# Performance work log

Measured on AMD Instinct MI355X. Metric: run time of the kernel, lower is better.

The kernel has to match this reference:

```python
import jax, jax.numpy as jnp
import numpy as np

MUL0, MUL1 = 128, 64            # scalar (0e) and vector (1o) multiplicities
B = 8192                        # batch of nodes
SQRT3 = 3.0 ** 0.5
SQRT6 = 6.0 ** 0.5

# path normalization (e3nn 'component' irrep norm / 'element' path norm):
# coeff_ins = sqrt(dim(ir_out) / fan_in(i_out)), fan_in = sum_{ins -> i_out} mul1*mul2
A_0E = (1.0 / (MUL0 * MUL0 + MUL1 * MUL1)) ** 0.5   # paths (0,0,0)+(1,1,0)
A_1O = (3.0 / (MUL0 * MUL1 + MUL1 * MUL0)) ** 0.5   # paths (0,1,1)+(1,0,1)
A_1E = (3.0 / (MUL1 * MUL1)) ** 0.5                  # path  (1,1,1)


def _levi_civita():
    eps = np.zeros((3, 3, 3), dtype=np.float32)
    eps[0, 1, 2] = eps[1, 2, 0] = eps[2, 0, 1] = 1.0
    eps[0, 2, 1] = eps[2, 1, 0] = eps[1, 0, 2] = -1.0
    return jnp.asarray(eps)


def setup_inputs() -> dict:
    key = jax.random.key(0)
    ks = jax.random.split(key, 7)
    return {
        "x1": jax.random.normal(ks[0], (B, MUL0 + 3 * MUL1), dtype=jnp.float32),
        "x2": jax.random.normal(ks[1], (B, MUL0 + 3 * MUL1), dtype=jnp.float32),
        "w000": jax.random.normal(ks[2], (MUL0, MUL0, MUL0), dtype=jnp.float32),
        "w011": jax.random.normal(ks[3], (MUL0, MUL1, MUL1), dtype=jnp.float32),
        "w101": jax.random.normal(ks[4], (MUL1, MUL0, MUL1), dtype=jnp.float32),
        "w110": jax.random.normal(ks[5], (MUL1, MUL1, MUL0), dtype=jnp.float32),
        "w111": jax.random.normal(ks[6], (MUL1, MUL1, MUL1), dtype=jnp.float32),
    }


def reference(x1, x2, w000, w011, w101, w110, w111):
    b = x1.shape[0]
    # split irreps: scalars [b, 128], vectors [b, 64, 3]
    s1, v1 = x1[:, :MUL0], x1[:, MUL0:].reshape(b, MUL1, 3)
    s2, v2 = x2[:, :MUL0], x2[:, MUL0:].reshape(b, MUL1, 3)

    # 0e output: 0e x 0e -> 0e (w3j = 1) and 1o x 1o -> 0e (w3j = delta/sqrt3)
    out0 = A_0E * (
        jnp.einsum("uvw,bu,bv->bw", w000, s1, s2)
        + jnp.einsum("uvw,bui,bvi->bw", w110, v1, v2) / SQRT3
    )

    # 1o output: 0e x 1o -> 1o and 1o x 0e -> 1o (w3j = delta/sqrt3)
    out1o = (A_1O / SQRT3) * (
        jnp.einsum("uvw,bu,bvi->bwi", w011, s1, v2)
        + jnp.einsum("uvw,bui,bv->bwi", w101, v1, s2)
    )

    # 1e output: 1o x 1o -> 1e (w3j = levi-civita / sqrt6)
    eps = _levi_civita()
    out1e = (A_1E / SQRT6) * jnp.einsum("uvw,bui,bvj,ijk->bwk", w111, v1, v2, eps)

    return jnp.concatenate(
        [out0, out1o.reshape(b, -1), out1e.reshape(b, -1)], axis=-1
    )  # [b, 128 + 192 + 192] = [b, 512]
```

## Files before the change

### kernel.cpp

```cpp
#include <hip/hip_runtime.h>
#include <stdint.h>


typedef _Float16 f16;
typedef f16 f16x8 __attribute__((ext_vector_type(8)));
typedef float f32x4 __attribute__((ext_vector_type(4)));
typedef int i32x4 __attribute__((ext_vector_type(4)));

#define OFF_W000 0u
#define OFF_W110 2097152u
#define OFF_W011 2621440u
#define OFF_W101 3145728u
#define OFF_W111 3670016u
#define OFF_XS1  3932160u
#define OFF_XS2  4980736u
#define OFF_XV1  6029312u
#define OFF_XV2  7602176u
#define OFF_S0A  9175040u
#define OFF_S0B  10223616u
#define OFF_S1O  13369344u
#define WS_ELEMS 14942208u

#define SC_0E 0.006987712429686843f
#define SC_1O 0.0078125f
#define SC_1E 0.011048543456039806f

__global__ void tile_weights_k(const float* __restrict__ w000, const float* __restrict__ w011,
                               const float* __restrict__ w101, const float* __restrict__ w110,
                               const float* __restrict__ w111, f16* __restrict__ ws)
{
  unsigned tid = blockIdx.x*256u + threadIdx.x;
  if (tid < 2097152u) {
    unsigned e=tid&7u, n=(tid>>3)&127u, q=(tid>>10)&3u, p=(tid>>12)&1u, u=(tid>>13)&127u, vh=(tid>>20)&1u;
    unsigned v = vh*64u + p*32u + q*8u + e;
    ws[OFF_W000+tid] = (f16)w000[u*16384u + v*128u + n];
    return;
  }
  tid -= 2097152u;
  if (tid < 524288u) {
    unsigned e=tid&7u, n=(tid>>3)&127u, q=(tid>>10)&3u, p=(tid>>12)&1u, u=tid>>13;
    unsigned v = p*32u + q*8u + e;
    ws[OFF_W110+tid] = (f16)(w110[u*8192u + v*128u + n] * 0.5773502691896258f);
    return;
  }
  tid -= 524288u;
  if (tid < 524288u) {
    unsigned e=tid&7u, n=(tid>>3)&63u, q=(tid>>9)&3u, p=(tid>>11)&1u, u=tid>>12;
    unsigned v = p*32u + q*8u + e;
    ws[OFF_W011+tid] = (f16)w011[u*4096u + v*64u + n];
    return;
  }
  tid -= 524288u;
  if (tid < 524288u) {
    unsigned e=tid&7u, n=(tid>>3)&63u, q=(tid>>9)&3u, p=(tid>>11)&1u, u=tid>>12;
    unsigned v = p*32u + q*8u + e;
    ws[OFF_W101+tid] = (f16)w101[v*8192u + u*64u + n];
    return;
  }
  tid -= 524288u;
  {
    unsigned e=tid&7u, n=(tid>>3)&63u, q=(tid>>9)&3u, p=(tid>>11)&1u, u=tid>>12;
    unsigned v = p*32u + q*8u + e;
    ws[OFF_W111+tid] = (f16)w111[u*4096u + v*64u + n];
  }
}

__global__ void tile_x_k(const float* __restrict__ x1, const float* __restrict__ x2,
                         f16* __restrict__ ws)
{
  unsigned tid = blockIdx.x*256u + threadIdx.x;
  if (tid < 1048576u) {
    unsigned e=tid&7u, r=(tid>>3)&127u, uo=(tid>>10)&15u, rt=tid>>14;
    ws[OFF_XS1+tid] = (f16)x1[(rt*128u+r)*320u + uo*8u + e];
    return;
  }
  tid -= 1048576u;
  if (tid < 1572864u) {
    unsigned e=tid&7u, r=(tid>>3)&127u, ov=(tid>>10)&7u, rest=tid>>13;
    unsigned i=rest%3u, rt=rest/3u;
    ws[OFF_XV1+tid] = (f16)x1[(rt*128u+r)*320u + 128u + (ov*8u+e)*3u + i];
    return;
  }
  tid -= 1572864u;
  if (tid < 1048576u) {
    unsigned e=tid&7u, r=(tid>>3)&127u, uo=(tid>>10)&15u, rt=tid>>14;
    ws[OFF_XS2+tid] = (f16)x2[(rt*128u+r)*320u + uo*8u + e];
    return;
  }
  tid -= 1048576u;
  {
    unsigned e=tid&7u, r=(tid>>3)&127u, ov=(tid>>10)&7u, rest=tid>>13;
    unsigned i=rest%3u, rt=rest/3u;
    ws[OFF_XV2+tid] = (f16)x2[(rt*128u+r)*320u + 128u + (ov*8u+e)*3u + i];
  }
}

#define GLD16(g,l) __builtin_amdgcn_global_load_lds( \
    (const __attribute__((address_space(1))) unsigned int*)(g), \
    (__attribute__((address_space(3))) unsigned int*)(l), 16, 0, 0)

#define WAITV(n) asm volatile("s_waitcnt vmcnt(" #n ")" ::: "memory")

template<int N, bool NEG>
__device__ __forceinline__ void run_phase(const f16* __restrict__ Wt, int supersteps,
    const f16* __restrict__ aW, const f16* __restrict__ bW, int bRow, int h,
    f16* sW, f16* sA, f32x4 (&acc)[4][4])
{
  constexpr int S = N/64;
  constexpr int TILE = N*32;
  const int lane = threadIdx.x & 63, wid = threadIdx.x >> 6;
  const int q = lane >> 4, r15 = lane & 15;
  const int steps = supersteps*16;

  f16x8 br[4][2];
#pragma unroll
  for (int mt=0; mt<4; ++mt)
#pragma unroll
    for (int o=0; o<2; ++o)
      br[mt][o] = *(const f16x8*)(bW + (o*4+q)*1024 + (bRow + mt*16 + r15)*8);
#pragma unroll
  for (int mt=0; mt<4; ++mt)
#pragma unroll
    for (int o=0; o<2; ++o) {
      i32x4 tmp = __builtin_bit_cast(i32x4, br[mt][o]);
      asm volatile("" :: "v"(tmp));
    }

  auto stW = [&](int t, int buf){
#pragma unroll
    for (int c=0;c<S;++c)
      GLD16((const char*)(Wt + t*TILE + (wid*S+c)*512) + lane*16,
            (char*)(sW + buf*4096 + (wid*S+c)*512));
  };
  auto stA = [&](int uo, int buf){
    GLD16((const char*)(aW + uo*1024) + lane*16, (char*)(sA + buf*512));
  };

  stW(0,0); stA(0,0); stW(1,1);
  asm volatile("s_waitcnt vmcnt(0)" ::: "memory");
  __builtin_amdgcn_s_barrier();
  __builtin_amdgcn_sched_barrier(0);

  int rb = 0;
  for (int ss = 0; ss < supersteps; ++ss) {
    const f16* ab = sA + (ss&1)*512;
#pragma unroll
    for (int p = 0; p < 16; ++p) {
      const int t = ss*16 + p;
      if (t + 2 < steps) {
        if (p >= 14) { if constexpr (S==1) WAITV(2); else WAITV(3); }
        else         { if constexpr (S==1) WAITV(1); else WAITV(2); }
      } else WAITV(0);
      __builtin_amdgcn_s_barrier();
      __builtin_amdgcn_sched_barrier(0);
      int wb = rb+2; if (wb>=3) wb-=3;
      if (t + 2 < steps) stW(t+2, wb);
      if (p == 13 && ss+1 < supersteps) stA(ss+1, (ss+1)&1);

      const int ul = p>>1, par = p&1;
      f16x8 af[4];
#pragma unroll
      for (int mt=0; mt<4; ++mt) {
        f16 av = ab[(mt*16+r15)*8 + ul];
        if constexpr (NEG) av = -av;
        af[mt] = av * br[mt][par];
      }
      const f16* W = sW + rb*4096;
#pragma unroll
      for (int nt=0; nt<4; ++nt) {
        f16x8 bw = *(const f16x8*)(W + (q*N + h*64 + nt*16 + r15)*8);
#pragma unroll
        for (int mt=0; mt<4; ++mt)
          acc[mt][nt] = __builtin_amdgcn_mfma_f32_16x16x32_f16(af[mt], bw, acc[mt][nt], 0,0,0);
      }
      rb = rb+1; if (rb>=3) rb-=3;
    }
  }
  __builtin_amdgcn_s_barrier();
  __builtin_amdgcn_sched_barrier(0);
}

__global__ __launch_bounds__(256, 3)
void tp_main(f16* __restrict__ ws, float* __restrict__ out)
{
  __shared__ f16 smem[16384];
  f16* sW = smem;
  const int lane = threadIdx.x & 63, wid = threadIdx.x >> 6;
  f16* sA = smem + 12288 + wid*1024;
  const int q = lane >> 4, r15 = lane & 15;

  f32x4 acc[4][4];
#pragma unroll
  for (int a=0;a<4;++a)
#pragma unroll
    for (int b=0;b<4;++b) acc[a][b] = (f32x4){0.f,0.f,0.f,0.f};

  const int bid = blockIdx.x;

  if (bid < 128) {
    const int rt = bid >> 1, vh = bid & 1;
    const int rgrp = wid >> 1, h = wid & 1;
    const f16* aW = ws + OFF_XS1 + rt*16384 + rgrp*512;
    const f16* bW = ws + OFF_XS2 + rt*16384 + vh*8192;
    run_phase<128,false>(ws + OFF_W000 + vh*1048576u, 16, aW, bW, rgrp*64, h, sW, sA, acc);
    const int rowb = rt*128 + rgrp*64;
    if (vh == 0) {
#pragma unroll
      for (int mt=0;mt<4;++mt)
#pragma unroll
        for (int nt=0;nt<4;++nt)
#pragma unroll
          for (int rg=0;rg<4;++rg)
            out[(rowb+mt*16+q*4+rg)*512 + h*64+nt*16+r15] = SC_0E*acc[mt][nt][rg];
    } else {
      f16* slab = ws + OFF_S0A;
#pragma unroll
      for (int mt=0;mt<4;++mt)
#pragma unroll
        for (int nt=0;nt<4;++nt)
#pragma unroll
          for (int rg=0;rg<4;++rg)
            slab[(rowb+mt*16+q*4+rg)*128 + h*64+nt*16+r15] = (f16)(SC_0E*acc[mt][nt][rg]);
    }
  } else if (bid < 224) {
    const int id = bid-128, i = id%3, rt = id/3;
    const int rgrp = wid, ro = rgrp & 1, sub = rgrp >> 1;
    const int rtt = rt*2 + sub;
    const f16* aW = ws + OFF_XS1 + rtt*16384 + ro*512;
    const f16* bW = ws + OFF_XV2 + (rtt*3+i)*8192;
    run_phase<64,false>(ws + OFF_W011, 16, aW, bW, ro*64, 0, sW, sA, acc);
    const int rowb = rt*256 + rgrp*64;
#pragma unroll
    for (int mt=0;mt<4;++mt)
#pragma unroll
      for (int nt=0;nt<4;++nt)
#pragma unroll
        for (int rg=0;rg<4;++rg)
          out[(rowb+mt*16+q*4+rg)*512 + 128 + 3*(nt*16+r15) + i] = SC_1O*acc[mt][nt][rg];
  } else if (bid < 320) {
    const int id = bid-224, i = id%3, rt = id/3;
    const int rgrp = wid, ro = rgrp & 1, sub = rgrp >> 1;
    const int rtt = rt*2 + sub;
    const f16* aW = ws + OFF_XS2 + rtt*16384 + ro*512;
    const f16* bW = ws + OFF_XV1 + (rtt*3+i)*8192;
    run_phase<64,false>(ws + OFF_W101, 16, aW, bW, ro*64, 0, sW, sA, acc);
    const int rowb = rt*256 + rgrp*64;
    f16* slab = ws + OFF_S1O;
#pragma unroll
    for (int mt=0;mt<4;++mt)
#pragma unroll
      for (int nt=0;nt<4;++nt)
#pragma unroll
        for (int rg=0;rg<4;++rg)
          slab[(rowb+mt*16+q*4+rg)*192 + 3*(nt*16+r15) + i] = (f16)(SC_1O*acc[mt][nt][rg]);
  } else if (bid < 416) {
    const int id = bid-320, kk = id%3, rt = id/3;
    int i = kk+1; if (i>2) i-=3;
    int j = kk+2; if (j>2) j-=3;
    const int rgrp = wid, ro = rgrp & 1, sub = rgrp >> 1;
    const int rtt = rt*2 + sub;
    run_phase<64,false>(ws + OFF_W111, 8,
        ws + OFF_XV1 + (rtt*3+i)*8192 + ro*512, ws + OFF_XV2 + (rtt*3+j)*8192,
        ro*64, 0, sW, sA, acc);
    run_phase<64,true>(ws + OFF_W111, 8,
        ws + OFF_XV1 + (rtt*3+j)*8192 + ro*512, ws + OFF_XV2 + (rtt*3+i)*8192,
        ro*64, 0, sW, sA, acc);
    const int rowb = rt*256 + rgrp*64;
#pragma unroll
    for (int mt=0;mt<4;++mt)
#pragma unroll
      for (int nt=0;nt<4;++nt)
#pragma unroll
        for (int rg=0;rg<4;++rg)
          out[(rowb+mt*16+q*4+rg)*512 + 320 + 3*(nt*16+r15) + kk] = SC_1E*acc[mt][nt][rg];
  } else {
    const int id = bid-416, i = id%3, rt = id/3;
    const int rgrp = wid >> 1, h = wid & 1;
    const f16* aW = ws + OFF_XV1 + (rt*3+i)*8192 + rgrp*512;
    const f16* bW = ws + OFF_XV2 + (rt*3+i)*8192;
    run_phase<128,false>(ws + OFF_W110, 8, aW, bW, rgrp*64, h, sW, sA, acc);
    const int rowb = rt*128 + rgrp*64;
    f16* slab = ws + OFF_S0B + (unsigned)i*1048576u;
#pragma unroll
    for (int mt=0;mt<4;++mt)
#pragma unroll
      for (int nt=0;nt<4;++nt)
#pragma unroll
        for (int rg=0;rg<4;++rg)
          slab[(rowb+mt*16+q*4+rg)*128 + h*64+nt*16+r15] = (f16)(SC_0E*acc[mt][nt][rg]);
  }
}

__global__ void ep_add(const f16* __restrict__ ws, float* __restrict__ out)
{
  unsigned tid = blockIdx.x*256u + threadIdx.x;
  if (tid < 1048576u) {
    unsigned r = tid>>7, c = tid&127u;
    float s = (float)ws[OFF_S0A+tid] + (float)ws[OFF_S0B+tid]
            + (float)ws[OFF_S0B+1048576u+tid] + (float)ws[OFF_S0B+2097152u+tid];
    out[r*512u+c] += s;
  } else {
    unsigned t2 = tid - 1048576u;
    unsigned r = t2/192u, c = t2 - r*192u;
    out[r*512u+128u+c] += (float)ws[OFF_S1O+t2];
  }
}

extern "C" void kernel_launch(void* const* d_in, const int* in_sizes, int n_in,
                              void* d_out, int out_size, void* d_ws, size_t ws_size,
                              hipStream_t stream)
{
  const float* x1   = (const float*)d_in[0];
  const float* x2   = (const float*)d_in[1];
  const float* w000 = (const float*)d_in[2];
  const float* w011 = (const float*)d_in[3];
  const float* w101 = (const float*)d_in[4];
  const float* w110 = (const float*)d_in[5];
  const float* w111 = (const float*)d_in[6];
  float* out = (float*)d_out;
  f16* ws   = (f16*)d_ws;

  if (ws_size < (size_t)WS_ELEMS * 2) return;

  tile_weights_k<<<15360, 256, 0, stream>>>(w000, w011, w101, w110, w111, ws);
  tile_x_k<<<20480, 256, 0, stream>>>(x1, x2, ws);
  tp_main<<<608, 256, 0, stream>>>(ws, out);
  ep_add<<<10240, 256, 0, stream>>>(ws, out);
}
```

Before: 161.4 us.

## Stage weight tiles in pairs with deeper LDS buffering and merge tiling kernels

The main tensor-product loop now loads two weight K-tiles per barrier into a four-slot LDS ring, which halves the number of barriers and wait points. Activation rows are read once per superstep into registers. LDS grows to 72KB, so occupancy drops from 3 to 2 blocks per CU. The 0e-from-vectors branch now processes two row tiles per block, cutting the grid from 608 to 512 blocks, and the two preprocessing kernels are merged into one launch. The cost is lower occupancy and a longer tail for the blocks that loop twice.

```diff
diff --git a/kernel.cpp b/kernel.cpp
--- a/kernel.cpp
+++ b/kernel.cpp
@@ -25,9 +25,10 @@
 #define SC_1O 0.0078125f
 #define SC_1E 0.011048543456039806f
 
-__global__ void tile_weights_k(const float* __restrict__ w000, const float* __restrict__ w011,
-                               const float* __restrict__ w101, const float* __restrict__ w110,
-                               const float* __restrict__ w111, f16* __restrict__ ws)
+__global__ void tile_all_k(const float* __restrict__ w000, const float* __restrict__ w011,
+                           const float* __restrict__ w101, const float* __restrict__ w110,
+                           const float* __restrict__ w111, const float* __restrict__ x1,
+                           const float* __restrict__ x2, f16* __restrict__ ws)
 {
   unsigned tid = blockIdx.x*256u + threadIdx.x;
   if (tid < 2097152u) {
@@ -58,17 +59,13 @@
     return;
   }
   tid -= 524288u;
-  {
+  if (tid < 262144u) {
     unsigned e=tid&7u, n=(tid>>3)&63u, q=(tid>>9)&3u, p=(tid>>11)&1u, u=tid>>12;
     unsigned v = p*32u + q*8u + e;
     ws[OFF_W111+tid] = (f16)w111[u*4096u + v*64u + n];
-  }
-}
-
-__global__ void tile_x_k(const float* __restrict__ x1, const float* __restrict__ x2,
-                         f16* __restrict__ ws)
-{
-  unsigned tid = blockIdx.x*256u + threadIdx.x;
+    return;
+  }
+  tid -= 262144u;
   if (tid < 1048576u) {
     unsigned e=tid&7u, r=(tid>>3)&127u, uo=(tid>>10)&15u, rt=tid>>14;
     ws[OFF_XS1+tid] = (f16)x1[(rt*128u+r)*320u + uo*8u + e];
@@ -101,16 +98,21 @@
 
 #define WAITV(n) asm volatile("s_waitcnt vmcnt(" #n ")" ::: "memory")
 
-template<int N, bool NEG>
-__device__ __forceinline__ void run_phase(const f16* __restrict__ Wt, int supersteps,
+template<int N, bool NEG, int SS>
+__device__ __forceinline__ void run_phase(const f16* __restrict__ Wt,
     const f16* __restrict__ aW, const f16* __restrict__ bW, int bRow, int h,
-    f16* sW, f16* sA, f32x4 (&acc)[4][4])
-{
-  constexpr int S = N/64;
-  constexpr int TILE = N*32;
+    f16* sW, f16* sAw, f32x4 (&acc)[4][4])
+{
+  constexpr int S     = N/64;
+  constexpr int TILEB = N*64;
+  constexpr int PAIRB = 2*TILEB;
+  constexpr int TILEE = N*32;
+  constexpr int PAIRE = 2*TILEE;
+  constexpr int M     = SS*8;
   const int lane = threadIdx.x & 63, wid = threadIdx.x >> 6;
   const int q = lane >> 4, r15 = lane & 15;
-  const int steps = supersteps*16;
+
+  WAITV(0);
 
   f16x8 br[4][2];
 #pragma unroll
@@ -126,67 +128,75 @@
       asm volatile("" :: "v"(tmp));
     }
 
-  auto stW = [&](int t, int buf){
-#pragma unroll
-    for (int c=0;c<S;++c)
-      GLD16((const char*)(Wt + t*TILE + (wid*S+c)*512) + lane*16,
-            (char*)(sW + buf*4096 + (wid*S+c)*512));
+  const int wchunk = wid*S*1024;
+  auto stPair = [&](int p, int slot){
+    const char* s = (const char*)Wt + (size_t)p*PAIRB + wchunk;
+    char* d = (char*)sW + slot*PAIRB + wchunk;
+#pragma unroll
+    for (int tt=0; tt<2; ++tt)
+#pragma unroll
+      for (int c=0; c<S; ++c)
+        GLD16(s + tt*TILEB + c*1024 + lane*16, d + tt*TILEB + c*1024);
   };
-  auto stA = [&](int uo, int buf){
-    GLD16((const char*)(aW + uo*1024) + lane*16, (char*)(sA + buf*512));
+  auto stA = [&](int ss2){
+    GLD16((const char*)(aW + ss2*1024) + lane*16, (char*)sAw + (ss2&1)*1024);
   };
 
-  stW(0,0); stA(0,0); stW(1,1);
-  asm volatile("s_waitcnt vmcnt(0)" ::: "memory");
+  stA(0); stPair(0,0); stPair(1,1);
+
+#pragma unroll 1
+  for (int ss = 0; ss < SS; ++ss) {
+    f16x8 aR[4];
+#pragma unroll
+    for (int k = 0; k < 8; ++k) {
+      const int m = ss*8 + k;
+      if (k == 7) {
+        if (ss+1 < SS) { if constexpr (S==1) WAITV(3); else WAITV(5); }
+        else           WAITV(0);
+      } else {
+        if constexpr (S==1) WAITV(2); else WAITV(4);
+      }
+      __builtin_amdgcn_s_barrier();
+      __builtin_amdgcn_sched_barrier(0);
+      if (k == 6 && ss+1 < SS) stA(ss+1);
+      if (m+2 < M) stPair(m+2, (k+2)&3);
+      if (k == 0) {
+#pragma unroll
+        for (int mt=0; mt<4; ++mt)
+          aR[mt] = *(const f16x8*)(sAw + (ss&1)*512 + (mt*16+r15)*8);
+      }
+      f16x8 af[4][2];
+#pragma unroll
+      for (int mt=0; mt<4; ++mt) {
+        f16 av = aR[mt][k];
+        if constexpr (NEG) av = -av;
+        af[mt][0] = av * br[mt][0];
+        af[mt][1] = av * br[mt][1];
+      }
+#pragma unroll
+      for (int tt=0; tt<2; ++tt) {
+        const f16* W = sW + (k&3)*PAIRE + tt*TILEE;
+#pragma unroll
+        for (int nt=0; nt<4; ++nt) {
+          f16x8 bw = *(const f16x8*)(W + (q*N + h*64 + nt*16 + r15)*8);
+#pragma unroll
+          for (int mt=0; mt<4; ++mt)
+            acc[mt][nt] = __builtin_amdgcn_mfma_f32_16x16x32_f16(af[mt][tt], bw, acc[mt][nt], 0,0,0);
+        }
+      }
+    }
+  }
   __builtin_amdgcn_s_barrier();
   __builtin_amdgcn_sched_barrier(0);
-
-  int rb = 0;
-  for (int ss = 0; ss < supersteps; ++ss) {
-    const f16* ab = sA + (ss&1)*512;
-#pragma unroll
-    for (int p = 0; p < 16; ++p) {
-      const int t = ss*16 + p;
-      if (t + 2 < steps) {
-        if (p >= 14) { if constexpr (S==1) WAITV(2); else WAITV(3); }
-        else         { if constexpr (S==1) WAITV(1); else WAITV(2); }
-      } else WAITV(0);
-      __builtin_amdgcn_s_barrier();
-      __builtin_amdgcn_sched_barrier(0);
-      int wb = rb+2; if (wb>=3) wb-=3;
-      if (t + 2 < steps) stW(t+2, wb);
-      if (p == 13 && ss+1 < supersteps) stA(ss+1, (ss+1)&1);
-
-      const int ul = p>>1, par = p&1;
-      f16x8 af[4];
-#pragma unroll
-      for (int mt=0; mt<4; ++mt) {
-        f16 av = ab[(mt*16+r15)*8 + ul];
-        if constexpr (NEG) av = -av;
-        af[mt] = av * br[mt][par];
-      }
-      const f16* W = sW + rb*4096;
-#pragma unroll
-      for (int nt=0; nt<4; ++nt) {
-        f16x8 bw = *(const f16x8*)(W + (q*N + h*64 + nt*16 + r15)*8);
-#pragma unroll
-        for (int mt=0; mt<4; ++mt)
-          acc[mt][nt] = __builtin_amdgcn_mfma_f32_16x16x32_f16(af[mt], bw, acc[mt][nt], 0,0,0);
-      }
-      rb = rb+1; if (rb>=3) rb-=3;
-    }
-  }
-  __builtin_amdgcn_s_barrier();
-  __builtin_amdgcn_sched_barrier(0);
-}
-
-__global__ __launch_bounds__(256, 3)
+}
+
+__global__ __launch_bounds__(256, 2)
 void tp_main(f16* __restrict__ ws, float* __restrict__ out)
 {
-  __shared__ f16 smem[16384];
+  __shared__ f16 smem[36864];
   f16* sW = smem;
   const int lane = threadIdx.x & 63, wid = threadIdx.x >> 6;
-  f16* sA = smem + 12288 + wid*1024;
+  f16* sAw = smem + 32768 + wid*1024;
   const int q = lane >> 4, r15 = lane & 15;
 
   f32x4 acc[4][4];
@@ -202,7 +212,7 @@
     const int rgrp = wid >> 1, h = wid & 1;
     const f16* aW = ws + OFF_XS1 + rt*16384 + rgrp*512;
     const f16* bW = ws + OFF_XS2 + rt*16384 + vh*8192;
-    run_phase<128,false>(ws + OFF_W000 + vh*1048576u, 16, aW, bW, rgrp*64, h, sW, sA, acc);
+    run_phase<128,false,16>(ws + OFF_W000 + vh*1048576u, aW, bW, rgrp*64, h, sW, sAw, acc);
     const int rowb = rt*128 + rgrp*64;
     if (vh == 0) {
 #pragma unroll
@@ -228,7 +238,7 @@
     const int rtt = rt*2 + sub;
     const f16* aW = ws + OFF_XS1 + rtt*16384 + ro*512;
     const f16* bW = ws + OFF_XV2 + (rtt*3+i)*8192;
-    run_phase<64,false>(ws + OFF_W011, 16, aW, bW, ro*64, 0, sW, sA, acc);
+    run_phase<64,false,16>(ws + OFF_W011, aW, bW, ro*64, 0, sW, sAw, acc);
     const int rowb = rt*256 + rgrp*64;
 #pragma unroll
     for (int mt=0;mt<4;++mt)
@@ -243,7 +253,7 @@
     const int rtt = rt*2 + sub;
     const f16* aW = ws + OFF_XS2 + rtt*16384 + ro*512;
     const f16* bW = ws + OFF_XV1 + (rtt*3+i)*8192;
-    run_phase<64,false>(ws + OFF_W101, 16, aW, bW, ro*64, 0, sW, sA, acc);
+    run_phase<64,false,16>(ws + OFF_W101, aW, bW, ro*64, 0, sW, sAw, acc);
     const int rowb = rt*256 + rgrp*64;
     f16* slab = ws + OFF_S1O;
 #pragma unroll
@@ -259,12 +269,12 @@
     int j = kk+2; if (j>2) j-=3;
     const int rgrp = wid, ro = rgrp & 1, sub = rgrp >> 1;
     const int rtt = rt*2 + sub;
-    run_phase<64,false>(ws + OFF_W111, 8,
+    run_phase<64,false,8>(ws + OFF_W111,
         ws + OFF_XV1 + (rtt*3+i)*8192 + ro*512, ws + OFF_XV2 + (rtt*3+j)*8192,
-        ro*64, 0, sW, sA, acc);
-    run_phase<64,true>(ws + OFF_W111, 8,
+        ro*64, 0, sW, sAw, acc);
+    run_phase<64,true,8>(ws + OFF_W111,
         ws + OFF_XV1 + (rtt*3+j)*8192 + ro*512, ws + OFF_XV2 + (rtt*3+i)*8192,
-        ro*64, 0, sW, sA, acc);
+        ro*64, 0, sW, sAw, acc);
     const int rowb = rt*256 + rgrp*64;
 #pragma unroll
     for (int mt=0;mt<4;++mt)
@@ -274,20 +284,26 @@
         for (int rg=0;rg<4;++rg)
           out[(rowb+mt*16+q*4+rg)*512 + 320 + 3*(nt*16+r15) + kk] = SC_1E*acc[mt][nt][rg];
   } else {
-    const int id = bid-416, i = id%3, rt = id/3;
+    const int id = bid-416, i = id%3, rp = id/3;
     const int rgrp = wid >> 1, h = wid & 1;
-    const f16* aW = ws + OFF_XV1 + (rt*3+i)*8192 + rgrp*512;
-    const f16* bW = ws + OFF_XV2 + (rt*3+i)*8192;
-    run_phase<128,false>(ws + OFF_W110, 8, aW, bW, rgrp*64, h, sW, sA, acc);
-    const int rowb = rt*128 + rgrp*64;
-    f16* slab = ws + OFF_S0B + (unsigned)i*1048576u;
-#pragma unroll
-    for (int mt=0;mt<4;++mt)
-#pragma unroll
-      for (int nt=0;nt<4;++nt)
-#pragma unroll
-        for (int rg=0;rg<4;++rg)
-          slab[(rowb+mt*16+q*4+rg)*128 + h*64+nt*16+r15] = (f16)(SC_0E*acc[mt][nt][rg]);
+#pragma unroll 1
+    for (int hh = 0; hh < 2; ++hh) {
+      const int rt = rp*2 + hh;
+      const f16* aW = ws + OFF_XV1 + (rt*3+i)*8192 + rgrp*512;
+      const f16* bW = ws + OFF_XV2 + (rt*3+i)*8192;
+      run_phase<128,false,8>(ws + OFF_W110, aW, bW, rgrp*64, h, sW, sAw, acc);
+      const int rowb = rt*128 + rgrp*64;
+      f16* slab = ws + OFF_S0B + (unsigned)i*1048576u;
+#pragma unroll
+      for (int mt=0;mt<4;++mt)
+#pragma unroll
+        for (int nt=0;nt<4;++nt)
+#pragma unroll
+          for (int rg=0;rg<4;++rg) {
+            slab[(rowb+mt*16+q*4+rg)*128 + h*64+nt*16+r15] = (f16)(SC_0E*acc[mt][nt][rg]);
+            acc[mt][nt][rg] = 0.f;
+          }
+    }
   }
 }
 
@@ -322,8 +338,7 @@
 
   if (ws_size < (size_t)WS_ELEMS * 2) return;
 
-  tile_weights_k<<<15360, 256, 0, stream>>>(w000, w011, w101, w110, w111, ws);
-  tile_x_k<<<20480, 256, 0, stream>>>(x1, x2, ws);
-  tp_main<<<608, 256, 0, stream>>>(ws, out);
+  tile_all_k<<<35840, 256, 0, stream>>>(w000, w011, w101, w110, w111, x1, x2, ws);
+  tp_main<<<512, 256, 0, stream>>>(ws, out);
   ep_add<<<10240, 256, 0, stream>>>(ws, out);
 }
```

Measured after the change: 149.2 us. -7.6%, faster.
